# Kernel optimization log

Hardware: AMD Instinct MI355X
Metric: run time of the kernel (lower is better)

## Reference

```python
import jax, jax.numpy as jnp
import numpy as np

N_NODES = 50000
N_EDGES = 1600000
S_FEAT, F_FEAT, HID, HEADS = 100, 200, 256, 8
HEAD_DIM = HID // HEADS


def setup_inputs() -> dict:
    key = jax.random.key(0)
    ks = jax.random.split(key, 8)
    inp = {
        "x": jax.random.normal(ks[0], (N_NODES, S_FEAT + F_FEAT), dtype=jnp.float32),
        "edge_index": jax.random.randint(ks[1], (2, N_EDGES), 0, N_NODES, dtype=jnp.int64),
        "W_s": jax.random.normal(ks[2], (S_FEAT, HID), dtype=jnp.float32) * (1.0 / np.sqrt(S_FEAT)),
        "b_s": jnp.zeros((HID,), jnp.float32),
        "W_f": jax.random.normal(ks[3], (F_FEAT, HID), dtype=jnp.float32) * (1.0 / np.sqrt(F_FEAT)),
        "b_f": jnp.zeros((HID,), jnp.float32),
        "in_proj_w": jax.random.normal(ks[4], (3 * HID, HID), dtype=jnp.float32) * (1.0 / np.sqrt(HID)),
        "in_proj_b": jnp.zeros((3 * HID,), jnp.float32),
        "out_proj_w": jax.random.normal(ks[5], (HID, HID), dtype=jnp.float32) * (1.0 / np.sqrt(HID)),
        "out_proj_b": jnp.zeros((HID,), jnp.float32),
        "out_w": jax.random.normal(ks[6], (1, HID), dtype=jnp.float32) * (1.0 / np.sqrt(HID)),
        "out_b": jnp.zeros((1,), jnp.float32),
    }
    return inp


def _gcn_conv(feat, W, b, src, dst, deg_inv, coef, n):
    # PyG GCNConv: h = feat @ W; out[i] = sum_j norm_ij * h_j + (1/deg_i) * h_i + b
    h = feat @ W  # [N, HID]
    agg = jax.ops.segment_sum(coef[:, None] * h[src], dst, num_segments=n)
    return agg + deg_inv[:, None] * h + b


def reference(x, edge_index, W_s, b_s, W_f, b_f,
              in_proj_w, in_proj_b, out_proj_w, out_proj_b, out_w, out_b):
    n = x.shape[0]
    src, dst = edge_index[0], edge_index[1]
    # symmetric GCN normalization with self-loops (edge weight 1)
    deg = 1.0 + jax.ops.segment_sum(jnp.ones(src.shape[0], x.dtype), dst, num_segments=n)
    deg_inv_sqrt = jax.lax.rsqrt(deg)
    coef = deg_inv_sqrt[src] * deg_inv_sqrt[dst]  # [E]
    deg_inv = deg_inv_sqrt * deg_inv_sqrt         # self-loop norm = 1/deg

    s = jax.nn.relu(_gcn_conv(x[:, :S_FEAT], W_s, b_s, src, dst, deg_inv, coef, n))
    f = jax.nn.relu(_gcn_conv(x[:, S_FEAT:S_FEAT + F_FEAT], W_f, b_f, src, dst, deg_inv, coef, n))

    comb = jnp.stack([s, f], axis=1)  # [N, 2, HID]
    qkv = comb @ in_proj_w.T + in_proj_b  # [N, 2, 3*HID]
    q, k, v = jnp.split(qkv, 3, axis=-1)
    def heads(t):  # [N, 2, HID] -> [N, H, 2, Dh]
        return t.reshape(n, 2, HEADS, HEAD_DIM).transpose(0, 2, 1, 3)
    q, k, v = heads(q), heads(k), heads(v)
    scores = jnp.einsum('nhqd,nhkd->nhqk', q, k) / np.sqrt(HEAD_DIM)
    attn = jax.nn.softmax(scores, axis=-1)
    o = jnp.einsum('nhqk,nhkd->nhqd', attn, v).transpose(0, 2, 1, 3).reshape(n, 2, HID)
    o = o @ out_proj_w.T + out_proj_b  # [N, 2, HID]

    fused = o.mean(axis=1)                 # [N, HID]
    pooled = fused.mean(axis=0, keepdims=True)  # [1, HID] (global_mean_pool, one graph)
    return (pooled @ out_w.T + out_b).squeeze(-1)  # [1]
```

## Files before the change

### kernel.cpp

```cpp
#include <hip/hip_runtime.h>
#include <hip/hip_bf16.h>
#include <math.h>

#define N_NODES 50000
#define N_EDGES 1600000
#define M_ROWS  100000

static const size_t XB_OFF   = 0;
static const size_t Y_OFF    = 32000000;
static const size_t CSR_OFF  = 64000000;
static const size_t COMB_OFF = 104000000;
static const size_t ROW_OFF  = 155200000;
static const size_t CNT_OFF  = 155400064;
static const size_t CUR_OFF  = 155600128;
static const size_t DIS_OFF  = 155800192;
static const size_t DINV_OFF = 156000256;
static const size_t BT_OFF   = 156200320;
static const size_t B2_OFF   = 156495232;
static const size_t WP_OFF   = 156497536;
static const size_t U_OFF    = 156498560;
static const size_t CH_OFF   = 156506752;
static const size_t FLAG_OFF = 156506816;
static const size_t ACC_OFF  = 156506880;
static const size_t WT2_OFF  = 156506944;
static const size_t WS_NEED  = 156834624;

typedef __attribute__((ext_vector_type(8))) short short8v;
typedef __attribute__((ext_vector_type(4))) float f32x4;

__device__ __forceinline__ float bf_lo(unsigned int u) { return __uint_as_float(u << 16); }
__device__ __forceinline__ float bf_hi(unsigned int u) { return __uint_as_float(u & 0xffff0000u); }
__device__ __forceinline__ float bf2f(unsigned short u) { return __uint_as_float((unsigned int)u << 16); }
__device__ __forceinline__ unsigned short f2bf(float f) {
    unsigned int x = __float_as_uint(f);
    return (unsigned short)((x + 0x7fffu + ((x >> 16) & 1u)) >> 16);
}


__global__ void k_guard(float* out) { if (threadIdx.x == 0) out[0] = -12345.0f; }

__global__ void k_detect(const int* __restrict__ raw, int* __restrict__ flag) {
    if (raw[2 * threadIdx.x + 1] != 0) atomicOr(flag, 1);
}

__device__ __forceinline__ void load_edge(const int* raw, int is32, int e, int& s, int& d) {
    if (is32) { s = raw[e]; d = raw[N_EDGES + e]; }
    else      { s = raw[2 * (size_t)e]; d = raw[2 * ((size_t)N_EDGES + e)]; }
}

__global__ __launch_bounds__(256) void k_deg(const int* __restrict__ raw,
                                             const int* __restrict__ flag,
                                             int* __restrict__ cnt) {
    int e = blockIdx.x * 256 + threadIdx.x;
    if (e >= N_EDGES) return;
    int s, d; load_edge(raw, *flag, e, s, d);
    atomicAdd(&cnt[d], 1);
}

__global__ __launch_bounds__(256) void k_norm(const int* __restrict__ cnt,
                                              float* __restrict__ dis, float* __restrict__ dinv) {
    int n = blockIdx.x * 256 + threadIdx.x;
    if (n < N_NODES) {
        float d = 1.0f + (float)cnt[n];
        float r = rsqrtf(d);
        dis[n]  = r;
        dinv[n] = r * r;
    }
}

__global__ __launch_bounds__(1024) void k_scan(const int* __restrict__ cnt,
                                               int* __restrict__ rowptr) {
    __shared__ int part[1024];
    const int CH = 49;
    int tid = threadIdx.x;
    int base = tid * CH;
    int s = 0;
    for (int i = 0; i < CH; ++i) {
        int idx = base + i;
        if (idx < N_NODES) s += cnt[idx];
    }
    part[tid] = s;
    __syncthreads();
    for (int off = 1; off < 1024; off <<= 1) {
        int v = (tid >= off) ? part[tid - off] : 0;
        __syncthreads();
        part[tid] += v;
        __syncthreads();
    }
    int excl = (tid == 0) ? 0 : part[tid - 1];
    for (int i = 0; i < CH; ++i) {
        int idx = base + i;
        if (idx < N_NODES) { rowptr[idx] = excl; excl += cnt[idx]; }
    }
    if (tid == 1023) rowptr[N_NODES] = excl;
}

__global__ __launch_bounds__(256) void k_place(const int* __restrict__ raw,
                                               const int* __restrict__ flag,
                                               const int* __restrict__ rowptr,
                                               int* __restrict__ cur,
                                               int* __restrict__ csr) {
    int e = blockIdx.x * 256 + threadIdx.x;
    if (e >= N_EDGES) return;
    int s, d; load_edge(raw, *flag, e, s, d);
    int pos = rowptr[d] + atomicAdd(&cur[d], 1);
    csr[pos] = s;
}

__global__ __launch_bounds__(256) void k_cvtx(const float* __restrict__ x,
                                              unsigned short* __restrict__ xb) {
    int idx = blockIdx.x * 256 + threadIdx.x;
    int row = idx / 80, g = idx - row * 80;
    if (row >= N_NODES) return;
    int c0 = g * 4;
    ushort4 o;
    if (c0 < 300) {
        float4 v = *reinterpret_cast<const float4*>(x + (size_t)row * 300 + c0);
        o.x = f2bf(v.x); o.y = f2bf(v.y); o.z = f2bf(v.z); o.w = f2bf(v.w);
    } else {
        o = make_ushort4(0, 0, 0, 0);
    }
    *reinterpret_cast<ushort4*>(xb + (size_t)row * 320 + c0) = o;
}

__global__ __launch_bounds__(256) void k_wt2(const float* __restrict__ Ws,
                                             const float* __restrict__ Wf,
                                             unsigned short* __restrict__ Wt2) {
    int j = blockIdx.x;
    for (int k = threadIdx.x; k < 320; k += 256) {
        float v = 0.0f;
        if (j < 256) { if (k < 100) v = Ws[(size_t)k * 256 + j]; }
        else         { if (k >= 100 && k < 300) v = Wf[(size_t)(k - 100) * 256 + (j - 256)]; }
        Wt2[(size_t)j * 320 + k] = f2bf(v);
    }
}

__global__ __launch_bounds__(256) void k_aggx(const int* __restrict__ csr,
                                              const int* __restrict__ rowptr,
                                              const float* __restrict__ dis,
                                              const float* __restrict__ dinv,
                                              const unsigned short* __restrict__ xb,
                                              unsigned short* __restrict__ y) {
    int n    = blockIdx.x * 4 + (threadIdx.x >> 6);
    int lane = threadIdx.x & 63;
    if (n >= N_NODES || lane >= 40) return;
    int beg = rowptr[n], end = rowptr[n + 1];
    float a0=0,a1=0,a2=0,a3=0,a4=0,a5=0,a6=0,a7=0;
    int e = beg;
    for (; e + 8 <= end; e += 8) {
        int s0 = csr[e],   s1 = csr[e+1], s2 = csr[e+2], s3 = csr[e+3];
        int s4 = csr[e+4], s5 = csr[e+5], s6 = csr[e+6], s7 = csr[e+7];
        float c0 = dis[s0], c1 = dis[s1], c2 = dis[s2], c3 = dis[s3];
        float c4 = dis[s4], c5 = dis[s5], c6 = dis[s6], c7 = dis[s7];
        uint4 v0 = *reinterpret_cast<const uint4*>(xb + (size_t)s0 * 320 + lane * 8);
        uint4 v1 = *reinterpret_cast<const uint4*>(xb + (size_t)s1 * 320 + lane * 8);
        uint4 v2 = *reinterpret_cast<const uint4*>(xb + (size_t)s2 * 320 + lane * 8);
        uint4 v3 = *reinterpret_cast<const uint4*>(xb + (size_t)s3 * 320 + lane * 8);
        uint4 v4 = *reinterpret_cast<const uint4*>(xb + (size_t)s4 * 320 + lane * 8);
        uint4 v5 = *reinterpret_cast<const uint4*>(xb + (size_t)s5 * 320 + lane * 8);
        uint4 v6 = *reinterpret_cast<const uint4*>(xb + (size_t)s6 * 320 + lane * 8);
        uint4 v7 = *reinterpret_cast<const uint4*>(xb + (size_t)s7 * 320 + lane * 8);
        a0 += c0*bf_lo(v0.x); a1 += c0*bf_hi(v0.x); a2 += c0*bf_lo(v0.y); a3 += c0*bf_hi(v0.y);
        a4 += c0*bf_lo(v0.z); a5 += c0*bf_hi(v0.z); a6 += c0*bf_lo(v0.w); a7 += c0*bf_hi(v0.w);
        a0 += c1*bf_lo(v1.x); a1 += c1*bf_hi(v1.x); a2 += c1*bf_lo(v1.y); a3 += c1*bf_hi(v1.y);
        a4 += c1*bf_lo(v1.z); a5 += c1*bf_hi(v1.z); a6 += c1*bf_lo(v1.w); a7 += c1*bf_hi(v1.w);
        a0 += c2*bf_lo(v2.x); a1 += c2*bf_hi(v2.x); a2 += c2*bf_lo(v2.y); a3 += c2*bf_hi(v2.y);
        a4 += c2*bf_lo(v2.z); a5 += c2*bf_hi(v2.z); a6 += c2*bf_lo(v2.w); a7 += c2*bf_hi(v2.w);
        a0 += c3*bf_lo(v3.x); a1 += c3*bf_hi(v3.x); a2 += c3*bf_lo(v3.y); a3 += c3*bf_hi(v3.y);
        a4 += c3*bf_lo(v3.z); a5 += c3*bf_hi(v3.z); a6 += c3*bf_lo(v3.w); a7 += c3*bf_hi(v3.w);
        a0 += c4*bf_lo(v4.x); a1 += c4*bf_hi(v4.x); a2 += c4*bf_lo(v4.y); a3 += c4*bf_hi(v4.y);
        a4 += c4*bf_lo(v4.z); a5 += c4*bf_hi(v4.z); a6 += c4*bf_lo(v4.w); a7 += c4*bf_hi(v4.w);
        a0 += c5*bf_lo(v5.x); a1 += c5*bf_hi(v5.x); a2 += c5*bf_lo(v5.y); a3 += c5*bf_hi(v5.y);
        a4 += c5*bf_lo(v5.z); a5 += c5*bf_hi(v5.z); a6 += c5*bf_lo(v5.w); a7 += c5*bf_hi(v5.w);
        a0 += c6*bf_lo(v6.x); a1 += c6*bf_hi(v6.x); a2 += c6*bf_lo(v6.y); a3 += c6*bf_hi(v6.y);
        a4 += c6*bf_lo(v6.z); a5 += c6*bf_hi(v6.z); a6 += c6*bf_lo(v6.w); a7 += c6*bf_hi(v6.w);
        a0 += c7*bf_lo(v7.x); a1 += c7*bf_hi(v7.x); a2 += c7*bf_lo(v7.y); a3 += c7*bf_hi(v7.y);
        a4 += c7*bf_lo(v7.z); a5 += c7*bf_hi(v7.z); a6 += c7*bf_lo(v7.w); a7 += c7*bf_hi(v7.w);
    }
    for (; e < end; ++e) {
        int s = csr[e];
        float c = dis[s];
        uint4 v = *reinterpret_cast<const uint4*>(xb + (size_t)s * 320 + lane * 8);
        a0 += c*bf_lo(v.x); a1 += c*bf_hi(v.x); a2 += c*bf_lo(v.y); a3 += c*bf_hi(v.y);
        a4 += c*bf_lo(v.z); a5 += c*bf_hi(v.z); a6 += c*bf_lo(v.w); a7 += c*bf_hi(v.w);
    }
    float dn = dis[n], di = dinv[n];
    uint4 hv = *reinterpret_cast<const uint4*>(xb + (size_t)n * 320 + lane * 8);
    float r0 = dn*a0 + di*bf_lo(hv.x);
    float r1 = dn*a1 + di*bf_hi(hv.x);
    float r2 = dn*a2 + di*bf_lo(hv.y);
    float r3 = dn*a3 + di*bf_hi(hv.y);
    float r4 = dn*a4 + di*bf_lo(hv.z);
    float r5 = dn*a5 + di*bf_hi(hv.z);
    float r6 = dn*a6 + di*bf_lo(hv.w);
    float r7 = dn*a7 + di*bf_hi(hv.w);
    uint4 o;
    o.x = (unsigned int)f2bf(r0) | ((unsigned int)f2bf(r1) << 16);
    o.y = (unsigned int)f2bf(r2) | ((unsigned int)f2bf(r3) << 16);
    o.z = (unsigned int)f2bf(r4) | ((unsigned int)f2bf(r5) << 16);
    o.w = (unsigned int)f2bf(r6) | ((unsigned int)f2bf(r7) << 16);
    *reinterpret_cast<uint4*>(y + (size_t)n * 320 + lane * 8) = o;
}

__global__ __launch_bounds__(256) void k_comb(const unsigned short* __restrict__ y,
                                              const unsigned short* __restrict__ Wt2,
                                              const float* __restrict__ bs,
                                              const float* __restrict__ bf,
                                              unsigned short* __restrict__ comb) {
    __shared__ __align__(16) unsigned short sA[64][40];
    __shared__ __align__(16) unsigned short sB[64][40];
    int tid  = threadIdx.x;
    int lane = tid & 63, wid = tid >> 6;
    int wm = wid >> 1, wn = wid & 1;
    int arow = tid >> 2, aseg = (tid & 3) * 8;
    int cblk = blockIdx.x, rblk = blockIdx.y;
    long grow = (long)rblk * 64 + arow;
    bool aval = grow < N_NODES;
    const unsigned short* aptr = y + grow * 320 + aseg;
    const unsigned short* bptr = Wt2 + ((long)cblk * 64 + arow) * 320 + aseg;

    f32x4 acc00 = {0,0,0,0}, acc01 = {0,0,0,0}, acc10 = {0,0,0,0}, acc11 = {0,0,0,0};
    int fr = lane & 15, fk = (lane >> 4) * 8;

    for (int ks = 0; ks < 10; ++ks) {
        uint4 av = aval ? *reinterpret_cast<const uint4*>(aptr + ks * 32) : make_uint4(0,0,0,0);
        uint4 bv = *reinterpret_cast<const uint4*>(bptr + ks * 32);
        __syncthreads();
        *reinterpret_cast<uint4*>(&sA[arow][aseg]) = av;
        *reinterpret_cast<uint4*>(&sB[arow][aseg]) = bv;
        __syncthreads();
        short8v a0 = *reinterpret_cast<const short8v*>(&sA[wm * 32 + fr][fk]);
        short8v a1 = *reinterpret_cast<const short8v*>(&sA[wm * 32 + 16 + fr][fk]);
        short8v b0 = *reinterpret_cast<const short8v*>(&sB[wn * 32 + fr][fk]);
        short8v b1 = *reinterpret_cast<const short8v*>(&sB[wn * 32 + 16 + fr][fk]);
        acc00 = __builtin_amdgcn_mfma_f32_16x16x32_bf16(a0, b0, acc00, 0, 0, 0);
        acc01 = __builtin_amdgcn_mfma_f32_16x16x32_bf16(a0, b1, acc01, 0, 0, 0);
        acc10 = __builtin_amdgcn_mfma_f32_16x16x32_bf16(a1, b0, acc10, 0, 0, 0);
        acc11 = __builtin_amdgcn_mfma_f32_16x16x32_bf16(a1, b1, acc11, 0, 0, 0);
    }

    int crow = rblk * 64 + wm * 32;
    int ccol = cblk * 64 + wn * 32;
    int rb = (lane >> 4) * 4;
    #pragma unroll
    for (int mn = 0; mn < 4; ++mn) {
        int m = mn >> 1, nn = mn & 1;
        f32x4 a = (mn == 0) ? acc00 : (mn == 1) ? acc01 : (mn == 2) ? acc10 : acc11;
        int col = ccol + nn * 16 + (lane & 15);
        int t  = col >> 8;
        int c2 = col & 255;
        float bias = t ? bf[c2] : bs[c2];
        #pragma unroll
        for (int j = 0; j < 4; ++j) {
            int row = crow + m * 16 + rb + j;
            if (row < N_NODES)
                comb[(size_t)(2 * row + t) * 256 + c2] = f2bf(fmaxf(a[j] + bias, 0.0f));
        }
    }
}

__global__ __launch_bounds__(256) void k_wprime(const float* __restrict__ ow,
                                                const float* __restrict__ opw,
                                                float* __restrict__ wp) {
    int i = threadIdx.x;
    float s = 0.0f;
    for (int j = 0; j < 256; ++j) s += ow[j] * opw[j * 256 + i];
    wp[i] = s;
}

__global__ __launch_bounds__(256) void k_u(const float* __restrict__ ipw,
                                           const float* __restrict__ ipb,
                                           const float* __restrict__ wp,
                                           float* __restrict__ u, float* __restrict__ ch) {
    int hd = blockIdx.x, i = threadIdx.x;
    float s = 0.0f;
    for (int d = 0; d < 32; ++d)
        s += ipw[(size_t)(512 + hd * 32 + d) * 256 + i] * wp[hd * 32 + d];
    u[hd * 256 + i] = s;
    if (i == 0) {
        float c = 0.0f;
        for (int d = 0; d < 32; ++d) c += ipb[512 + hd * 32 + d] * wp[hd * 32 + d];
        ch[hd] = c;
    }
}

__global__ __launch_bounds__(256) void k_makeB(const float* __restrict__ ipw,
                                               const float* __restrict__ ipb,
                                               const float* __restrict__ u,
                                               const float* __restrict__ ch,
                                               unsigned short* __restrict__ Bt,
                                               float* __restrict__ b2) {
    int j = blockIdx.x, k = threadIdx.x;
    float v = 0.0f;
    if (j < 512)      v = ipw[(size_t)j * 256 + k];
    else if (j < 520) v = u[(j - 512) * 256 + k];
    Bt[(size_t)j * 256 + k] = f2bf(v);
    if (k == 0) b2[j] = (j < 512) ? ipb[j] : ((j < 520) ? ch[j - 512] : 0.0f);
}

#define CT_STRIDE 546
__global__ __launch_bounds__(256) void k_fuse(const unsigned short* __restrict__ comb,
                                              const unsigned short* __restrict__ Bt,
                                              const float* __restrict__ b2,
                                              double* __restrict__ accum) {
    __shared__ __align__(16) unsigned short CT[64 * CT_STRIDE];
    __shared__ __align__(16) unsigned short sA[64][40];
    __shared__ __align__(16) unsigned short sB[64][40];
    __shared__ float red[256];

    int tid  = threadIdx.x;
    int lane = tid & 63, wid = tid >> 6;
    int wm = wid >> 1, wn = wid & 1;
    int arow = tid >> 2, aseg = (tid & 3) * 8;
    long grow = (long)blockIdx.x * 64 + arow;
    bool aval = grow < M_ROWS;
    const unsigned short* aptr = comb + grow * 256 + aseg;
    int fr = lane & 15, fk = (lane >> 4) * 8;
    int rb = (lane >> 4) * 4;

    for (int cb = 0; cb < 9; ++cb) {
        const unsigned short* bptr = Bt + ((long)cb * 64 + arow) * 256 + aseg;
        f32x4 acc00 = {0,0,0,0}, acc01 = {0,0,0,0}, acc10 = {0,0,0,0}, acc11 = {0,0,0,0};
        for (int ks = 0; ks < 8; ++ks) {
            uint4 av = aval ? *reinterpret_cast<const uint4*>(aptr + ks * 32) : make_uint4(0,0,0,0);
            uint4 bv = *reinterpret_cast<const uint4*>(bptr + ks * 32);
            __syncthreads();
            *reinterpret_cast<uint4*>(&sA[arow][aseg]) = av;
            *reinterpret_cast<uint4*>(&sB[arow][aseg]) = bv;
            __syncthreads();
            short8v a0 = *reinterpret_cast<const short8v*>(&sA[wm * 32 + fr][fk]);
            short8v a1 = *reinterpret_cast<const short8v*>(&sA[wm * 32 + 16 + fr][fk]);
            short8v b0 = *reinterpret_cast<const short8v*>(&sB[wn * 32 + fr][fk]);
            short8v b1 = *reinterpret_cast<const short8v*>(&sB[wn * 32 + 16 + fr][fk]);
            acc00 = __builtin_amdgcn_mfma_f32_16x16x32_bf16(a0, b0, acc00, 0, 0, 0);
            acc01 = __builtin_amdgcn_mfma_f32_16x16x32_bf16(a0, b1, acc01, 0, 0, 0);
            acc10 = __builtin_amdgcn_mfma_f32_16x16x32_bf16(a1, b0, acc10, 0, 0, 0);
            acc11 = __builtin_amdgcn_mfma_f32_16x16x32_bf16(a1, b1, acc11, 0, 0, 0);
        }
        int ccol = cb * 64 + wn * 32;
        #pragma unroll
        for (int mn = 0; mn < 4; ++mn) {
            int m = mn >> 1, nn = mn & 1;
            f32x4 a = (mn == 0) ? acc00 : (mn == 1) ? acc01 : (mn == 2) ? acc10 : acc11;
            int col = ccol + nn * 16 + (lane & 15);
            if (col < 520) {
                float bias = b2[col];
                int rbase = wm * 32 + m * 16 + rb;
                #pragma unroll
                for (int j = 0; j < 4; ++j)
                    CT[(rbase + j) * CT_STRIDE + col] = f2bf(a[j] + bias);
            }
        }
    }
    __syncthreads();

    float acc = 0.0f;
    #pragma unroll
    for (int ii = 0; ii < 2; ++ii) {
        int it = tid + ii * 256;
        int node32 = it >> 4;
        int rem = it & 15, hd = rem >> 1, t = rem & 1;
        int gnode = blockIdx.x * 32 + node32;
        if (gnode < N_NODES) {
            const unsigned short* qr = &CT[(2 * node32 + t) * CT_STRIDE];
            const unsigned short* k0 = &CT[(2 * node32 + 0) * CT_STRIDE];
            const unsigned short* k1 = &CT[(2 * node32 + 1) * CT_STRIDE];
            const unsigned int* qw  = reinterpret_cast<const unsigned int*>(qr + hd * 32);
            const unsigned int* k0w = reinterpret_cast<const unsigned int*>(k0 + 256 + hd * 32);
            const unsigned int* k1w = reinterpret_cast<const unsigned int*>(k1 + 256 + hd * 32);
            float s0 = 0.0f, s1 = 0.0f;
            #pragma unroll
            for (int dw = 0; dw < 16; ++dw) {
                unsigned int qv = qw[dw], v0 = k0w[dw], v1 = k1w[dw];
                float ql = bf_lo(qv), qh = bf_hi(qv);
                s0 += ql * bf_lo(v0) + qh * bf_hi(v0);
                s1 += ql * bf_lo(v1) + qh * bf_hi(v1);
            }
            const float sc = 0.17677669529663687f;
            s0 *= sc; s1 *= sc;
            float m = fmaxf(s0, s1);
            float e0 = expf(s0 - m), e1 = expf(s1 - m);
            float inv = 1.0f / (e0 + e1);
            float vw0 = bf2f(k0[512 + hd]);
            float vw1 = bf2f(k1[512 + hd]);
            acc += (e0 * vw0 + e1 * vw1) * inv;
        }
    }
    red[tid] = acc;
    __syncthreads();
    for (int s = 128; s > 0; s >>= 1) {
        if (tid < s) red[tid] += red[tid + s];
        __syncthreads();
    }
    if (tid == 0) atomicAdd(accum, (double)red[0]);
}

__global__ __launch_bounds__(256) void k_final(const float* __restrict__ ow,
                                               const float* __restrict__ opb,
                                               const float* __restrict__ ob,
                                               const double* __restrict__ accum,
                                               float* __restrict__ out) {
    __shared__ float red[256];
    int tid = threadIdx.x;
    red[tid] = ow[tid] * opb[tid];
    __syncthreads();
    for (int s = 128; s > 0; s >>= 1) {
        if (tid < s) red[tid] += red[tid + s];
        __syncthreads();
    }
    if (tid == 0)
        out[0] = (float)(accum[0] / (2.0 * N_NODES) + (double)red[0] + (double)ob[0]);
}

extern "C" void kernel_launch(void* const* d_in, const int* in_sizes, int n_in,
                              void* d_out, int out_size, void* d_ws, size_t ws_size,
                              hipStream_t stream) {
    const float* x   = (const float*)d_in[0];
    const int*   ei  = (const int*)d_in[1];
    const float* Ws  = (const float*)d_in[2];
    const float* bs  = (const float*)d_in[3];
    const float* Wf  = (const float*)d_in[4];
    const float* bf  = (const float*)d_in[5];
    const float* ipw = (const float*)d_in[6];
    const float* ipb = (const float*)d_in[7];
    const float* opw = (const float*)d_in[8];
    const float* opb = (const float*)d_in[9];
    const float* ow  = (const float*)d_in[10];
    const float* ob  = (const float*)d_in[11];
    float* out = (float*)d_out;

    if (ws_size < WS_NEED) { k_guard<<<1, 64, 0, stream>>>(out); return; }

    char* ws = (char*)d_ws;
    unsigned short* xb   = (unsigned short*)(ws + XB_OFF);
    unsigned short* y    = (unsigned short*)(ws + Y_OFF);
    int*            csr  = (int*)           (ws + CSR_OFF);
    unsigned short* comb = (unsigned short*)(ws + COMB_OFF);
    int*            row  = (int*)           (ws + ROW_OFF);
    int*            cnt  = (int*)           (ws + CNT_OFF);
    int*            cur  = (int*)           (ws + CUR_OFF);
    float*          dis  = (float*)         (ws + DIS_OFF);
    float*          dinv = (float*)         (ws + DINV_OFF);
    unsigned short* Bt   = (unsigned short*)(ws + BT_OFF);
    float*          b2   = (float*)         (ws + B2_OFF);
    float*          wp   = (float*)         (ws + WP_OFF);
    float*          u    = (float*)         (ws + U_OFF);
    float*          chv  = (float*)         (ws + CH_OFF);
    int*            flag = (int*)           (ws + FLAG_OFF);
    double*         accum= (double*)        (ws + ACC_OFF);
    unsigned short* Wt2  = (unsigned short*)(ws + WT2_OFF);

    hipMemsetAsync(cnt,   0, (size_t)N_NODES * 4, stream);
    hipMemsetAsync(cur,   0, (size_t)N_NODES * 4, stream);
    hipMemsetAsync(flag,  0, 4, stream);
    hipMemsetAsync(accum, 0, 8, stream);

    k_detect<<<1, 256, 0, stream>>>(ei, flag);
    k_deg   <<<(N_EDGES + 255) / 256, 256, 0, stream>>>(ei, flag, cnt);
    k_norm  <<<(N_NODES + 255) / 256, 256, 0, stream>>>(cnt, dis, dinv);
    k_scan  <<<1, 1024, 0, stream>>>(cnt, row);
    k_place <<<(N_EDGES + 255) / 256, 256, 0, stream>>>(ei, flag, row, cur, csr);

    k_cvtx<<<(N_NODES * 80 + 255) / 256, 256, 0, stream>>>(x, xb);
    k_wt2 <<<512, 256, 0, stream>>>(Ws, Wf, Wt2);

    k_aggx<<<(N_NODES + 3) / 4, 256, 0, stream>>>(csr, row, dis, dinv, xb, y);

    k_wprime<<<1,   256, 0, stream>>>(ow, opw, wp);
    k_u     <<<8,   256, 0, stream>>>(ipw, ipb, wp, u, chv);
    k_makeB <<<576, 256, 0, stream>>>(ipw, ipb, u, chv, Bt, b2);

    dim3 gc(8, (N_NODES + 63) / 64);
    k_comb<<<gc, 256, 0, stream>>>(y, Wt2, bs, bf, comb);

    k_fuse<<<(M_ROWS + 63) / 64, 256, 0, stream>>>(comb, Bt, b2, accum);
    k_final<<<1, 256, 0, stream>>>(ow, opb, ob, accum, out);
}
```

Baseline: 743.2 us.

## Stage full A tile in LDS once and read B fragments directly from global

```diff
diff --git a/kernel.cpp b/kernel.cpp
--- a/kernel.cpp
+++ b/kernel.cpp
@@ -299,45 +299,49 @@
 }
 
 #define CT_STRIDE 546
+#define A_STRIDE  264
 __global__ __launch_bounds__(256) void k_fuse(const unsigned short* __restrict__ comb,
                                               const unsigned short* __restrict__ Bt,
                                               const float* __restrict__ b2,
                                               double* __restrict__ accum) {
+    __shared__ __align__(16) unsigned short A_lds[64 * A_STRIDE];
     __shared__ __align__(16) unsigned short CT[64 * CT_STRIDE];
-    __shared__ __align__(16) unsigned short sA[64][40];
-    __shared__ __align__(16) unsigned short sB[64][40];
     __shared__ float red[256];
 
     int tid  = threadIdx.x;
     int lane = tid & 63, wid = tid >> 6;
     int wm = wid >> 1, wn = wid & 1;
-    int arow = tid >> 2, aseg = (tid & 3) * 8;
-    long grow = (long)blockIdx.x * 64 + arow;
-    bool aval = grow < M_ROWS;
-    const unsigned short* aptr = comb + grow * 256 + aseg;
     int fr = lane & 15, fk = (lane >> 4) * 8;
     int rb = (lane >> 4) * 4;
 
+    for (int i = tid; i < 64 * 32; i += 256) {
+        int r = i >> 5, c8 = (i & 31) * 8;
+        long gr = (long)blockIdx.x * 64 + r;
+        uint4 v = (gr < M_ROWS) ? *reinterpret_cast<const uint4*>(comb + gr * 256 + c8)
+                                : make_uint4(0, 0, 0, 0);
+        *reinterpret_cast<uint4*>(&A_lds[r * A_STRIDE + c8]) = v;
+    }
+    __syncthreads();
+
+    const unsigned short* a0base = &A_lds[(wm * 32 + fr) * A_STRIDE + fk];
+    const unsigned short* a1base = a0base + 16 * A_STRIDE;
+
     for (int cb = 0; cb < 9; ++cb) {
-        const unsigned short* bptr = Bt + ((long)cb * 64 + arow) * 256 + aseg;
+        int ccol = cb * 64 + wn * 32;
+        const unsigned short* b0p = Bt + (size_t)(ccol + fr) * 256 + fk;
+        const unsigned short* b1p = b0p + 16 * 256;
         f32x4 acc00 = {0,0,0,0}, acc01 = {0,0,0,0}, acc10 = {0,0,0,0}, acc11 = {0,0,0,0};
+        #pragma unroll
         for (int ks = 0; ks < 8; ++ks) {
-            uint4 av = aval ? *reinterpret_cast<const uint4*>(aptr + ks * 32) : make_uint4(0,0,0,0);
-            uint4 bv = *reinterpret_cast<const uint4*>(bptr + ks * 32);
-            __syncthreads();
-            *reinterpret_cast<uint4*>(&sA[arow][aseg]) = av;
-            *reinterpret_cast<uint4*>(&sB[arow][aseg]) = bv;
-            __syncthreads();
-            short8v a0 = *reinterpret_cast<const short8v*>(&sA[wm * 32 + fr][fk]);
-            short8v a1 = *reinterpret_cast<const short8v*>(&sA[wm * 32 + 16 + fr][fk]);
-            short8v b0 = *reinterpret_cast<const short8v*>(&sB[wn * 32 + fr][fk]);
-            short8v b1 = *reinterpret_cast<const short8v*>(&sB[wn * 32 + 16 + fr][fk]);
+            short8v a0 = *reinterpret_cast<const short8v*>(a0base + ks * 32);
+            short8v a1 = *reinterpret_cast<const short8v*>(a1base + ks * 32);
+            short8v b0 = *reinterpret_cast<const short8v*>(b0p + ks * 32);
+            short8v b1 = *reinterpret_cast<const short8v*>(b1p + ks * 32);
             acc00 = __builtin_amdgcn_mfma_f32_16x16x32_bf16(a0, b0, acc00, 0, 0, 0);
             acc01 = __builtin_amdgcn_mfma_f32_16x16x32_bf16(a0, b1, acc01, 0, 0, 0);
             acc10 = __builtin_amdgcn_mfma_f32_16x16x32_bf16(a1, b0, acc10, 0, 0, 0);
             acc11 = __builtin_amdgcn_mfma_f32_16x16x32_bf16(a1, b1, acc11, 0, 0, 0);
         }
-        int ccol = cb * 64 + wn * 32;
         #pragma unroll
         for (int mn = 0; mn < 4; ++mn) {
             int m = mn >> 1, nn = mn & 1;
```

Result: no change. 752.9 us (+1.3%).
